# Kernel tuning notes

Hardware: AMD Instinct MI355X
Metric: run time of the kernel (lower is better)

The kernel has to match this reference:

```python
import jax, jax.numpy as jnp
import numpy as np

D_MODEL = 1024
N_HEADS = 16
D_HEAD = D_MODEL // N_HEADS
SCALE = 1.0 / float(np.sqrt(D_HEAD))


def setup_inputs() -> dict:
    key = jax.random.key(0)
    ks = jax.random.split(key, 6)
    B, T = 4, 2048
    x = jax.random.normal(ks[0], (B, T, D_MODEL), dtype=jnp.float32)
    # torch Linear weights are [out, in]; y = x @ W.T
    s = 1.0 / np.sqrt(D_MODEL)
    Wq = jax.random.uniform(ks[1], (D_MODEL, D_MODEL), jnp.float32, -s, s)
    Wk = jax.random.uniform(ks[2], (D_MODEL, D_MODEL), jnp.float32, -s, s)
    Wv = jax.random.uniform(ks[3], (D_MODEL, D_MODEL), jnp.float32, -s, s)
    Wo = jax.random.uniform(ks[4], (D_MODEL, D_MODEL), jnp.float32, -s, s)
    bo = jax.random.uniform(ks[5], (D_MODEL,), jnp.float32, -s, s)
    return {"x": x, "Wq": Wq, "Wk": Wk, "Wv": Wv, "Wo": Wo, "bo": bo}


def reference(x, Wq, Wk, Wv, Wo, bo):
    B, T, D = x.shape
    # QKV projections (torch Linear: x @ W.T), split into heads -> [B, H, T, d]
    def heads(y):
        return y.reshape(B, T, N_HEADS, D_HEAD).transpose(0, 2, 1, 3)
    q = heads(x @ Wq.T)
    k = heads(x @ Wk.T)
    v = heads(x @ Wv.T)
    scores = jnp.einsum("bhqd,bhkd->bhqk", q, k) * SCALE  # [B,H,T,T]
    probs = jax.nn.softmax(scores, axis=-1)
    # dropout is identity in eval/inference mode
    out = jnp.einsum("bhqk,bhkd->bhqd", probs, v)  # [B,H,T,d]
    out = out.transpose(0, 2, 1, 3).reshape(B, T, D)
    return out @ Wo.T + bo
```

## Files before the change

### kernel.cpp

```cpp
#include <hip/hip_runtime.h>
#include <stdint.h>

#define D_MODEL 1024
#define NH 16
#define DH 64
#define TSEQ 2048
#define BATCH 4
#define MTOT (BATCH*TSEQ)
#define NQ (MTOT*D_MODEL)
#define WSZ (D_MODEL*D_MODEL)
#define QSCALE 0.18033688f

typedef __attribute__((ext_vector_type(8))) short bf16x8;
typedef __attribute__((ext_vector_type(8))) unsigned short u16x8;
typedef __attribute__((ext_vector_type(4))) float f32x4;
typedef __attribute__((ext_vector_type(2))) float f32x2;
typedef unsigned short u16;
typedef unsigned int u32;

__device__ __forceinline__ void gl_lds16(const void* g, void* l) {
  __builtin_amdgcn_global_load_lds(
      (__attribute__((address_space(1))) void*)g,
      (__attribute__((address_space(3))) void*)l, 16, 0, 0);
}
__device__ __forceinline__ u16 f2bf(float f) {
  u32 u = __builtin_bit_cast(u32, f);
  u = u + 0x7fffu + ((u >> 16) & 1u);
  return (u16)(u >> 16);
}
__device__ __forceinline__ float bf2f(u16 b) {
  u32 u = ((u32)b) << 16;
  return __builtin_bit_cast(float, u);
}

__device__ __forceinline__ void exp2pk4(const f32x4 s, float& e0, float& e1,
                                        float& e2, float& e3, u32& pk01,
                                        u32& pk23) {
  asm("v_exp_f32 %0, %6\n\t"
      "v_exp_f32 %1, %7\n\t"
      "v_exp_f32 %2, %8\n\t"
      "v_exp_f32 %3, %9\n\t"
      "s_nop 1\n\t"
      "v_cvt_pk_bf16_f32 %4, %0, %1\n\t"
      "v_cvt_pk_bf16_f32 %5, %2, %3"
      : "=&v"(e0), "=&v"(e1), "=&v"(e2), "=&v"(e3), "=&v"(pk01), "=&v"(pk23)
      : "v"(s[0]), "v"(s[1]), "v"(s[2]), "v"(s[3]));
}

__global__ __launch_bounds__(256) void detect_dtype(
    const u32* __restrict__ wq_raw, int* __restrict__ flag)
{
  __shared__ int cnt;
  if (threadIdx.x == 0) cnt = 0;
  __syncthreads();
  int c = 0;
  for (int i = threadIdx.x; i < 2048; i += 256) {
    const u32 e = (wq_raw[i] >> 7) & 0xFFu;
    if (e >= 90u && e <= 126u) ++c;
  }
  atomicAdd(&cnt, c);
  __syncthreads();
  if (threadIdx.x == 0) *flag = (cnt > 1024) ? 1 : 0;
}

__global__ __launch_bounds__(256) void convert_inputs(
    const void* __restrict__ x, const void* __restrict__ wq,
    const void* __restrict__ wk, const void* __restrict__ wv,
    const void* __restrict__ wo,
    u16* __restrict__ xb, u16* __restrict__ wqb, u16* __restrict__ wkb,
    u16* __restrict__ wvb, u16* __restrict__ wob,
    const int* __restrict__ flag_p)
{
  const int flag = *flag_p;
  const int seg = blockIdx.y;
  const void* src; u16* dst; int n;
  switch (seg) {
    case 0:  src = x;  dst = xb;  n = NQ;  break;
    case 1:  src = wq; dst = wqb; n = WSZ; break;
    case 2:  src = wk; dst = wkb; n = WSZ; break;
    case 3:  src = wv; dst = wvb; n = WSZ; break;
    default: src = wo; dst = wob; n = WSZ; break;
  }
  if (flag && seg == 0) return;
  const int idx = (blockIdx.x * 256 + threadIdx.x) * 8;
  if (idx >= n) return;
  if (flag) {
    *(u16x8*)(dst + idx) = *(const u16x8*)((const u16*)src + idx);
  } else {
    const float4 f0 = *(const float4*)((const float*)src + idx);
    const float4 f1 = *(const float4*)((const float*)src + idx + 4);
    union { u16 s[8]; u16x8 v; } u;
    u.s[0] = f2bf(f0.x); u.s[1] = f2bf(f0.y); u.s[2] = f2bf(f0.z); u.s[3] = f2bf(f0.w);
    u.s[4] = f2bf(f1.x); u.s[5] = f2bf(f1.y); u.s[6] = f2bf(f1.z); u.s[7] = f2bf(f1.w);
    *(u16x8*)(dst + idx) = u.v;
  }
}

__global__ __launch_bounds__(256) void qkv_gemm(
    const int* __restrict__ flag_p, const u16* __restrict__ x_raw,
    u16* __restrict__ dout,
    const u16* __restrict__ Wq, const u16* __restrict__ Wk,
    const u16* __restrict__ Wv,
    u16* __restrict__ Ko, u16* __restrict__ VTo)
{
  __shared__ __align__(16) u16 As[2 * 128 * 32];
  __shared__ __align__(16) u16 Bs[2 * 128 * 32];
  const int flag = *flag_p;
  const u16* __restrict__ X = flag ? x_raw : dout;
  u16* __restrict__ QTo = flag ? dout : dout + NQ;
  const int t = threadIdx.x;
  const int z = blockIdx.z;
  const u16* __restrict__ W = (z == 0) ? Wq : (z == 1) ? Wk : Wv;
  const int m0 = blockIdx.x * 128;
  const int n0 = blockIdx.y * 128;
  const int wave = t >> 6, lane = t & 63;
  const int wm = (wave >> 1) * 64, wn = (wave & 1) * 64;
  const int lr = lane & 15, kg = (lane >> 4) * 8;

  const int srow0 = t >> 2, skc = (t & 3) * 8;
  const int srow1 = srow0 + 64;
  const u16* a0 = X + (size_t)(m0 + srow0) * D_MODEL + skc;
  const u16* a1 = X + (size_t)(m0 + srow1) * D_MODEL + skc;
  const u16* b0 = W + (size_t)(n0 + srow0) * D_MODEL + skc;
  const u16* b1 = W + (size_t)(n0 + srow1) * D_MODEL + skc;

  f32x4 acc[4][4] = {};

  for (int kt = 0; kt < D_MODEL / 64; ++kt) {
    gl_lds16(a0,      &As[t * 8]);
    gl_lds16(a1,      &As[(t + 256) * 8]);
    gl_lds16(a0 + 32, &As[4096 + t * 8]);
    gl_lds16(a1 + 32, &As[4096 + (t + 256) * 8]);
    gl_lds16(b0,      &Bs[t * 8]);
    gl_lds16(b1,      &Bs[(t + 256) * 8]);
    gl_lds16(b0 + 32, &Bs[4096 + t * 8]);
    gl_lds16(b1 + 32, &Bs[4096 + (t + 256) * 8]);
    a0 += 64; a1 += 64; b0 += 64; b1 += 64;
    __syncthreads();
#pragma unroll
    for (int h = 0; h < 2; ++h) {
      bf16x8 af[4], bfr[4];
#pragma unroll
      for (int i = 0; i < 4; ++i)
        af[i] = *(const bf16x8*)&As[h * 4096 + (wm + i * 16 + lr) * 32 + kg];
#pragma unroll
      for (int j = 0; j < 4; ++j)
        bfr[j] = *(const bf16x8*)&Bs[h * 4096 + (wn + j * 16 + lr) * 32 + kg];
#pragma unroll
      for (int i = 0; i < 4; ++i)
#pragma unroll
        for (int j = 0; j < 4; ++j)
          acc[i][j] = __builtin_amdgcn_mfma_f32_16x16x32_bf16(af[i], bfr[j], acc[i][j], 0, 0, 0);
    }
    __syncthreads();
  }

  const int bidx = m0 >> 11;
  if (z == 1) {
#pragma unroll
    for (int i = 0; i < 4; ++i) {
      const int rowg = m0 + wm + i * 16 + ((lane >> 4) << 2);
      const int tq = rowg & (TSEQ - 1);
#pragma unroll
      for (int j = 0; j < 4; ++j) {
        const int colg = n0 + wn + j * 16 + lr;
        const int h = colg >> 6, d = colg & 63;
        u16* dst = Ko + ((size_t)(bidx * NH + h) * TSEQ + tq) * DH + d;
#pragma unroll
        for (int r = 0; r < 4; ++r)
          dst[(size_t)r * DH] = f2bf(acc[i][j][r]);
      }
    }
  } else {
    u16* O = (z == 0) ? QTo : VTo;
    const float sc = (z == 0) ? QSCALE : 1.0f;
#pragma unroll
    for (int i = 0; i < 4; ++i) {
      const int rowg = m0 + wm + i * 16 + ((lane >> 4) << 2);
      const int tq = rowg & (TSEQ - 1);
#pragma unroll
      for (int j = 0; j < 4; ++j) {
        const int colg = n0 + wn + j * 16 + lr;
        const int h = colg >> 6, d = colg & 63;
        union { u16 s[4]; uint2 v; } u;
#pragma unroll
        for (int r = 0; r < 4; ++r) u.s[r] = f2bf(acc[i][j][r] * sc);
        *(uint2*)&O[((size_t)(bidx * NH + h) * DH + d) * TSEQ + tq] = u.v;
      }
    }
  }
}

__global__ __launch_bounds__(256) void flash_attn(
    const int* __restrict__ flag_p, const u16* __restrict__ dout,
    const u16* __restrict__ K, const u16* __restrict__ VT,
    u16* __restrict__ AO)
{
  __shared__ __align__(16) u16 Ks[2][2 * 64 * 32];
  __shared__ __align__(16) u16 Vs[2][2 * 64 * 32];
  __shared__ __align__(16) u16 Ps[4 * 64 * 72];
  __shared__ float Ls[4 * 64];
  const int flag = *flag_p;
  const u16* __restrict__ QT = flag ? dout : dout + NQ;
  const int t = threadIdx.x;
  const int wave = t >> 6, lane = t & 63;
  const int lr = lane & 15, g = lane >> 4, kg = g * 8;
  const int bh = blockIdx.x;
  const int q0 = blockIdx.y * 256;
  const u16* __restrict__ QTh = QT + (size_t)bh * DH * TSEQ;
  const u16* __restrict__ Kh = K + (size_t)bh * TSEQ * DH;
  const u16* __restrict__ Vh = VT + (size_t)bh * DH * TSEQ;

  const int qi = q0 + wave * 64 + lr;
  bf16x8 qf[8];
#pragma unroll
  for (int s = 0; s < 4; ++s) {
    union { u16 v[8]; bf16x8 b; } u0, u1;
#pragma unroll
    for (int j = 0; j < 8; ++j) {
      u0.v[j] = QTh[(size_t)(kg + j) * TSEQ + qi + s * 16];
      u1.v[j] = QTh[(size_t)(32 + kg + j) * TSEQ + qi + s * 16];
    }
    qf[s * 2] = u0.b; qf[s * 2 + 1] = u1.b;
  }

  f32x4 acc[4][4] = {};
  f32x2 ls0[4] = {}, ls1[4] = {};

  const int srow = t >> 2, skc = (t & 3) * 8;
  const u16* kb = Kh + (size_t)srow * DH + skc;
  const u16* vb = Vh + (size_t)srow * TSEQ + skc;
  u16* const pw = &Ps[wave * 64 * 72];

  gl_lds16(kb,      &Ks[0][t * 8]);
  gl_lds16(kb + 32, &Ks[0][(t + 256) * 8]);
  gl_lds16(vb,      &Vs[0][t * 8]);
  gl_lds16(vb + 32, &Vs[0][(t + 256) * 8]);
  kb += 64 * DH; vb += 64;

  int cur = 0;
  for (int j0 = 0; j0 < TSEQ; j0 += 64) {
    __syncthreads();
    if (j0 + 64 < TSEQ) {
      gl_lds16(kb,      &Ks[cur ^ 1][t * 8]);
      gl_lds16(kb + 32, &Ks[cur ^ 1][(t + 256) * 8]);
      gl_lds16(vb,      &Vs[cur ^ 1][t * 8]);
      gl_lds16(vb + 32, &Vs[cur ^ 1][(t + 256) * 8]);
      kb += 64 * DH; vb += 64;
    }
    const u16* __restrict__ Kc = Ks[cur];
    const u16* __restrict__ Vc = Vs[cur];

#pragma unroll
    for (int jn = 0; jn < 4; ++jn) {
      const bf16x8 kf0 = *(const bf16x8*)&Kc[(jn * 16 + lr) * 32 + kg];
      const bf16x8 kf1 = *(const bf16x8*)&Kc[2048 + (jn * 16 + lr) * 32 + kg];
#pragma unroll
      for (int s = 0; s < 4; ++s) {
        f32x4 sS = {};
        sS = __builtin_amdgcn_mfma_f32_16x16x32_bf16(kf0, qf[s * 2],     sS, 0, 0, 0);
        sS = __builtin_amdgcn_mfma_f32_16x16x32_bf16(kf1, qf[s * 2 + 1], sS, 0, 0, 0);
        float e0, e1, e2, e3;
        uint2 w;
        exp2pk4(sS, e0, e1, e2, e3, w.x, w.y);
        ls0[s] += (f32x2){e0, e1};
        ls1[s] += (f32x2){e2, e3};
        *(uint2*)&pw[s * 16 * 72 + lr * 72 + jn * 16 + g * 4] = w;
      }
    }

    bf16x8 pf0[4], pf1[4];
#pragma unroll
    for (int s = 0; s < 4; ++s) {
      pf0[s] = *(const bf16x8*)&pw[s * 16 * 72 + lr * 72 + kg];
      pf1[s] = *(const bf16x8*)&pw[s * 16 * 72 + lr * 72 + 32 + kg];
    }
#pragma unroll
    for (int dn = 0; dn < 4; ++dn) {
      const bf16x8 vf0 = *(const bf16x8*)&Vc[(dn * 16 + lr) * 32 + kg];
      const bf16x8 vf1 = *(const bf16x8*)&Vc[2048 + (dn * 16 + lr) * 32 + kg];
#pragma unroll
      for (int s = 0; s < 4; ++s) {
        acc[s][dn] = __builtin_amdgcn_mfma_f32_16x16x32_bf16(pf0[s], vf0, acc[s][dn], 0, 0, 0);
        acc[s][dn] = __builtin_amdgcn_mfma_f32_16x16x32_bf16(pf1[s], vf1, acc[s][dn], 0, 0, 0);
      }
    }
    cur ^= 1;
  }

#pragma unroll
  for (int s = 0; s < 4; ++s) {
    float l = (ls0[s][0] + ls0[s][1]) + (ls1[s][0] + ls1[s][1]);
    l += __shfl_xor(l, 16, 64);
    l += __shfl_xor(l, 32, 64);
    Ls[wave * 64 + s * 16 + lr] = l;
  }
  __syncthreads();

  const int bb = bh >> 4, hh = bh & 15;
#pragma unroll
  for (int s = 0; s < 4; ++s) {
#pragma unroll
    for (int r = 0; r < 4; ++r) {
      const int qq = g * 4 + r;
      const float inv = 1.f / fmaxf(Ls[wave * 64 + s * 16 + qq], 1e-30f);
      const int ti = q0 + wave * 64 + s * 16 + qq;
      u16* dst = AO + (((size_t)bb * TSEQ + ti) * NH + hh) * DH + lr;
#pragma unroll
      for (int dn = 0; dn < 4; ++dn)
        dst[dn * 16] = f2bf(acc[s][dn][r] * inv);
    }
  }
}

__global__ __launch_bounds__(256) void out_gemm(
    const int* __restrict__ flag_p,
    const u16* __restrict__ A, const u16* __restrict__ W,
    const void* __restrict__ bias_raw, void* __restrict__ outp)
{
  __shared__ __align__(16) u16 As[2 * 128 * 32];
  __shared__ __align__(16) u16 Bs[2 * 128 * 32];
  const int flag = *flag_p;
  const int t = threadIdx.x;
  const int m0 = blockIdx.x * 128;
  const int n0 = blockIdx.y * 128;
  const int wave = t >> 6, lane = t & 63;
  const int wm = (wave >> 1) * 64, wn = (wave & 1) * 64;
  const int lr = lane & 15, kg = (lane >> 4) * 8;

  const int srow0 = t >> 2, skc = (t & 3) * 8;
  const int srow1 = srow0 + 64;
  const u16* a0 = A + (size_t)(m0 + srow0) * D_MODEL + skc;
  const u16* a1 = A + (size_t)(m0 + srow1) * D_MODEL + skc;
  const u16* b0 = W + (size_t)(n0 + srow0) * D_MODEL + skc;
  const u16* b1 = W + (size_t)(n0 + srow1) * D_MODEL + skc;

  f32x4 acc[4][4] = {};

  for (int kt = 0; kt < D_MODEL / 64; ++kt) {
    gl_lds16(a0,      &As[t * 8]);
    gl_lds16(a1,      &As[(t + 256) * 8]);
    gl_lds16(a0 + 32, &As[4096 + t * 8]);
    gl_lds16(a1 + 32, &As[4096 + (t + 256) * 8]);
    gl_lds16(b0,      &Bs[t * 8]);
    gl_lds16(b1,      &Bs[(t + 256) * 8]);
    gl_lds16(b0 + 32, &Bs[4096 + t * 8]);
    gl_lds16(b1 + 32, &Bs[4096 + (t + 256) * 8]);
    a0 += 64; a1 += 64; b0 += 64; b1 += 64;
    __syncthreads();
#pragma unroll
    for (int h = 0; h < 2; ++h) {
      bf16x8 af[4], bfr[4];
#pragma unroll
      for (int i = 0; i < 4; ++i)
        af[i] = *(const bf16x8*)&As[h * 4096 + (wm + i * 16 + lr) * 32 + kg];
#pragma unroll
      for (int j = 0; j < 4; ++j)
        bfr[j] = *(const bf16x8*)&Bs[h * 4096 + (wn + j * 16 + lr) * 32 + kg];
#pragma unroll
      for (int i = 0; i < 4; ++i)
#pragma unroll
        for (int j = 0; j < 4; ++j)
          acc[i][j] = __builtin_amdgcn_mfma_f32_16x16x32_bf16(af[i], bfr[j], acc[i][j], 0, 0, 0);
    }
    __syncthreads();
  }

#pragma unroll
  for (int j = 0; j < 4; ++j) {
    const int colg = n0 + wn + j * 16 + lr;
    const float bv = flag ? bf2f(((const u16*)bias_raw)[colg])
                          : ((const float*)bias_raw)[colg];
#pragma unroll
    for (int i = 0; i < 4; ++i) {
      const int rowg = m0 + wm + i * 16 + ((lane >> 4) << 2);
      if (flag) {
        u16* dst = (u16*)outp + (size_t)rowg * D_MODEL + colg;
#pragma unroll
        for (int r = 0; r < 4; ++r)
          dst[(size_t)r * D_MODEL] = f2bf(acc[i][j][r] + bv);
      } else {
        float* dst = (float*)outp + (size_t)rowg * D_MODEL + colg;
#pragma unroll
        for (int r = 0; r < 4; ++r)
          dst[(size_t)r * D_MODEL] = acc[i][j][r] + bv;
      }
    }
  }
}

extern "C" void kernel_launch(void* const* d_in, const int* in_sizes, int n_in,
                              void* d_out, int out_size, void* d_ws, size_t ws_size,
                              hipStream_t stream) {
  const void* x  = d_in[0];
  const void* wq = d_in[1];
  const void* wk = d_in[2];
  const void* wv = d_in[3];
  const void* wo = d_in[4];
  const void* bo = d_in[5];
  u16* dout = (u16*)d_out;

  int* flag = (int*)d_ws;
  u16* wqb = (u16*)d_ws + 8;
  u16* wkb = wqb + WSZ;
  u16* wvb = wkb + WSZ;
  u16* wob = wvb + WSZ;
  u16* kk  = wob + WSZ;
  u16* vt  = kk + NQ;
  u16* ao  = vt + NQ;

  detect_dtype<<<1, 256, 0, stream>>>((const u32*)wq, flag);

  dim3 gc(NQ / (256 * 8), 5);
  convert_inputs<<<gc, dim3(256), 0, stream>>>(
      x, wq, wk, wv, wo, dout, wqb, wkb, wvb, wob, flag);

  dim3 g1(MTOT / 128, D_MODEL / 128, 3);
  qkv_gemm<<<g1, dim3(256), 0, stream>>>(
      flag, (const u16*)x, dout, wqb, wkb, wvb, kk, vt);

  dim3 g2(BATCH * NH, TSEQ / 256, 1);
  flash_attn<<<g2, dim3(256), 0, stream>>>(flag, dout, kk, vt, ao);

  dim3 g3(MTOT / 128, D_MODEL / 128, 1);
  out_gemm<<<g3, dim3(256), 0, stream>>>(flag, ao, wob, bo, d_out);
}
```

Before: 290.1 us.

## Interleave QK and PV MFMA phases, remap GEMM block order, skip bf16 weight copies

```diff
diff --git a/kernel.cpp b/kernel.cpp
--- a/kernel.cpp
+++ b/kernel.cpp
@@ -71,7 +71,7 @@
     u16* __restrict__ wvb, u16* __restrict__ wob,
     const int* __restrict__ flag_p)
 {
-  const int flag = *flag_p;
+  if (*flag_p) return;
   const int seg = blockIdx.y;
   const void* src; u16* dst; int n;
   switch (seg) {
@@ -81,19 +81,14 @@
     case 3:  src = wv; dst = wvb; n = WSZ; break;
     default: src = wo; dst = wob; n = WSZ; break;
   }
-  if (flag && seg == 0) return;
   const int idx = (blockIdx.x * 256 + threadIdx.x) * 8;
   if (idx >= n) return;
-  if (flag) {
-    *(u16x8*)(dst + idx) = *(const u16x8*)((const u16*)src + idx);
-  } else {
-    const float4 f0 = *(const float4*)((const float*)src + idx);
-    const float4 f1 = *(const float4*)((const float*)src + idx + 4);
-    union { u16 s[8]; u16x8 v; } u;
-    u.s[0] = f2bf(f0.x); u.s[1] = f2bf(f0.y); u.s[2] = f2bf(f0.z); u.s[3] = f2bf(f0.w);
-    u.s[4] = f2bf(f1.x); u.s[5] = f2bf(f1.y); u.s[6] = f2bf(f1.z); u.s[7] = f2bf(f1.w);
-    *(u16x8*)(dst + idx) = u.v;
-  }
+  const float4 f0 = *(const float4*)((const float*)src + idx);
+  const float4 f1 = *(const float4*)((const float*)src + idx + 4);
+  union { u16 s[8]; u16x8 v; } u;
+  u.s[0] = f2bf(f0.x); u.s[1] = f2bf(f0.y); u.s[2] = f2bf(f0.z); u.s[3] = f2bf(f0.w);
+  u.s[4] = f2bf(f1.x); u.s[5] = f2bf(f1.y); u.s[6] = f2bf(f1.z); u.s[7] = f2bf(f1.w);
+  *(u16x8*)(dst + idx) = u.v;
 }
 
 __global__ __launch_bounds__(256) void qkv_gemm(
@@ -101,6 +96,8 @@
     u16* __restrict__ dout,
     const u16* __restrict__ Wq, const u16* __restrict__ Wk,
     const u16* __restrict__ Wv,
+    const void* __restrict__ wq_r, const void* __restrict__ wk_r,
+    const void* __restrict__ wv_r,
     u16* __restrict__ Ko, u16* __restrict__ VTo)
 {
   __shared__ __align__(16) u16 As[2 * 128 * 32];
@@ -110,8 +107,12 @@
   u16* __restrict__ QTo = flag ? dout : dout + NQ;
   const int t = threadIdx.x;
   const int z = blockIdx.z;
-  const u16* __restrict__ W = (z == 0) ? Wq : (z == 1) ? Wk : Wv;
-  const int m0 = blockIdx.x * 128;
+  const u16* __restrict__ Wc = (z == 0) ? Wq : (z == 1) ? Wk : Wv;
+  const u16* __restrict__ Wr = (const u16*)((z == 0) ? wq_r : (z == 1) ? wk_r : wv_r);
+  const u16* __restrict__ W = flag ? Wr : Wc;
+  const int bx = blockIdx.x;
+  const int mb = ((bx & 7) << 3) | (bx >> 3);
+  const int m0 = mb * 128;
   const int n0 = blockIdx.y * 128;
   const int wave = t >> 6, lane = t & 63;
   const int wm = (wave >> 1) * 64, wn = (wave & 1) * 64;
@@ -252,7 +253,7 @@
     const u16* __restrict__ Vc = Vs[cur];
 
 #pragma unroll
-    for (int jn = 0; jn < 4; ++jn) {
+    for (int jn = 0; jn < 2; ++jn) {
       const bf16x8 kf0 = *(const bf16x8*)&Kc[(jn * 16 + lr) * 32 + kg];
       const bf16x8 kf1 = *(const bf16x8*)&Kc[2048 + (jn * 16 + lr) * 32 + kg];
 #pragma unroll
@@ -269,21 +270,47 @@
       }
     }
 
-    bf16x8 pf0[4], pf1[4];
-#pragma unroll
-    for (int s = 0; s < 4; ++s) {
+    bf16x8 pf0[4];
+#pragma unroll
+    for (int s = 0; s < 4; ++s)
       pf0[s] = *(const bf16x8*)&pw[s * 16 * 72 + lr * 72 + kg];
-      pf1[s] = *(const bf16x8*)&pw[s * 16 * 72 + lr * 72 + 32 + kg];
-    }
+
+#pragma unroll
+    for (int jn = 2; jn < 4; ++jn) {
+      const bf16x8 kf0 = *(const bf16x8*)&Kc[(jn * 16 + lr) * 32 + kg];
+      const bf16x8 kf1 = *(const bf16x8*)&Kc[2048 + (jn * 16 + lr) * 32 + kg];
+#pragma unroll
+      for (int s = 0; s < 4; ++s) {
+        f32x4 sS = {};
+        sS = __builtin_amdgcn_mfma_f32_16x16x32_bf16(kf0, qf[s * 2],     sS, 0, 0, 0);
+        sS = __builtin_amdgcn_mfma_f32_16x16x32_bf16(kf1, qf[s * 2 + 1], sS, 0, 0, 0);
+        float e0, e1, e2, e3;
+        uint2 w;
+        exp2pk4(sS, e0, e1, e2, e3, w.x, w.y);
+        ls0[s] += (f32x2){e0, e1};
+        ls1[s] += (f32x2){e2, e3};
+        *(uint2*)&pw[s * 16 * 72 + lr * 72 + jn * 16 + g * 4] = w;
+      }
+    }
+
 #pragma unroll
     for (int dn = 0; dn < 4; ++dn) {
       const bf16x8 vf0 = *(const bf16x8*)&Vc[(dn * 16 + lr) * 32 + kg];
+#pragma unroll
+      for (int s = 0; s < 4; ++s)
+        acc[s][dn] = __builtin_amdgcn_mfma_f32_16x16x32_bf16(pf0[s], vf0, acc[s][dn], 0, 0, 0);
+    }
+
+    bf16x8 pf1[4];
+#pragma unroll
+    for (int s = 0; s < 4; ++s)
+      pf1[s] = *(const bf16x8*)&pw[s * 16 * 72 + lr * 72 + 32 + kg];
+#pragma unroll
+    for (int dn = 0; dn < 4; ++dn) {
       const bf16x8 vf1 = *(const bf16x8*)&Vc[2048 + (dn * 16 + lr) * 32 + kg];
 #pragma unroll
-      for (int s = 0; s < 4; ++s) {
-        acc[s][dn] = __builtin_amdgcn_mfma_f32_16x16x32_bf16(pf0[s], vf0, acc[s][dn], 0, 0, 0);
+      for (int s = 0; s < 4; ++s)
         acc[s][dn] = __builtin_amdgcn_mfma_f32_16x16x32_bf16(pf1[s], vf1, acc[s][dn], 0, 0, 0);
-      }
     }
     cur ^= 1;
   }
@@ -316,13 +343,17 @@
 __global__ __launch_bounds__(256) void out_gemm(
     const int* __restrict__ flag_p,
     const u16* __restrict__ A, const u16* __restrict__ W,
+    const void* __restrict__ wo_r,
     const void* __restrict__ bias_raw, void* __restrict__ outp)
 {
   __shared__ __align__(16) u16 As[2 * 128 * 32];
   __shared__ __align__(16) u16 Bs[2 * 128 * 32];
   const int flag = *flag_p;
+  const u16* __restrict__ Wm = flag ? (const u16*)wo_r : W;
   const int t = threadIdx.x;
-  const int m0 = blockIdx.x * 128;
+  const int bx = blockIdx.x;
+  const int mb = ((bx & 7) << 3) | (bx >> 3);
+  const int m0 = mb * 128;
   const int n0 = blockIdx.y * 128;
   const int wave = t >> 6, lane = t & 63;
   const int wm = (wave >> 1) * 64, wn = (wave & 1) * 64;
@@ -332,8 +363,8 @@
   const int srow1 = srow0 + 64;
   const u16* a0 = A + (size_t)(m0 + srow0) * D_MODEL + skc;
   const u16* a1 = A + (size_t)(m0 + srow1) * D_MODEL + skc;
-  const u16* b0 = W + (size_t)(n0 + srow0) * D_MODEL + skc;
-  const u16* b1 = W + (size_t)(n0 + srow1) * D_MODEL + skc;
+  const u16* b0 = Wm + (size_t)(n0 + srow0) * D_MODEL + skc;
+  const u16* b1 = Wm + (size_t)(n0 + srow1) * D_MODEL + skc;
 
   f32x4 acc[4][4] = {};
 
@@ -417,11 +448,11 @@
 
   dim3 g1(MTOT / 128, D_MODEL / 128, 3);
   qkv_gemm<<<g1, dim3(256), 0, stream>>>(
-      flag, (const u16*)x, dout, wqb, wkb, wvb, kk, vt);
+      flag, (const u16*)x, dout, wqb, wkb, wvb, wq, wk, wv, kk, vt);
 
   dim3 g2(BATCH * NH, TSEQ / 256, 1);
   flash_attn<<<g2, dim3(256), 0, stream>>>(flag, dout, kk, vt, ao);
 
   dim3 g3(MTOT / 128, D_MODEL / 128, 1);
-  out_gemm<<<g3, dim3(256), 0, stream>>>(flag, ao, wob, bo, d_out);
-}
+  out_gemm<<<g3, dim3(256), 0, stream>>>(flag, ao, wob, wo, bo, d_out);
+}
```

After: 287.7 us. About the same (-0.8%).
